# Optimization experiments

Measured on AMD Instinct MI355X. Metric: run time of the kernel, lower is better.

The kernel has to match this reference:

```python
import jax, jax.numpy as jnp
import numpy as np

N_NODES = 100000
N_EDGES = 800000
HIDDEN = 128
BN_EPS = 1e-5


def setup_inputs() -> dict:
    key = jax.random.key(0)
    k1, k2, k3 = jax.random.split(key, 3)
    x = jax.random.normal(k1, (N_NODES, HIDDEN), dtype=jnp.float32)
    edge_index = jax.random.randint(k2, (2, N_EDGES), 0, N_NODES, dtype=jnp.int64)
    # Glorot-style init for the GCN linear weight
    W = jax.random.normal(k3, (HIDDEN, HIDDEN), dtype=jnp.float32) / np.sqrt(HIDDEN)
    b = jnp.zeros((HIDDEN,), dtype=jnp.float32)
    gamma = jnp.ones((HIDDEN,), dtype=jnp.float32)
    beta = jnp.zeros((HIDDEN,), dtype=jnp.float32)
    return {"x": x, "edge_index": edge_index, "W": W, "b": b, "gamma": gamma, "beta": beta}


def reference(x, edge_index, W, b, gamma, beta):
    N = x.shape[0]
    xw = x @ W  # [N, d] linear transform first (PyG order)

    # add self-loops
    loops = jnp.arange(N, dtype=edge_index.dtype)
    row = jnp.concatenate([edge_index[0], loops])  # source
    col = jnp.concatenate([edge_index[1], loops])  # target

    # symmetric degree normalization on A~ = A + I
    deg = jax.ops.segment_sum(jnp.ones_like(col, dtype=x.dtype), col, num_segments=N)
    dinv = jax.lax.rsqrt(jnp.maximum(deg, 1.0))  # deg >= 1 due to self-loops
    norm = dinv[row] * dinv[col]  # [E+N]

    # gather -> scale -> scatter-add aggregation
    msgs = xw[row] * norm[:, None]  # [E+N, d]
    agg = jax.ops.segment_sum(msgs, col, num_segments=N) + b  # [N, d]

    # BatchNorm1d (batch statistics, biased variance) + ReLU; Dropout is identity (eval)
    mean = jnp.mean(agg, axis=0)
    var = jnp.var(agg, axis=0)
    h = (agg - mean) * jax.lax.rsqrt(var + BN_EPS) * gamma + beta
    return jax.nn.relu(h)
```

## Files before the change

### kernel.cpp

```cpp
#include <hip/hip_runtime.h>
#include <cstddef>

#define HIDDEN 128
#define BN_EPS 1e-5f
#define KS 136
#define BKT 64

typedef __attribute__((ext_vector_type(8))) short short8;
typedef __attribute__((ext_vector_type(4))) float float4v;
typedef __attribute__((ext_vector_type(4))) unsigned uint4v;

__device__ inline unsigned bf16_rne(float f) {
    unsigned u = __float_as_uint(f);
    return (u + 0x7fff + ((u >> 16) & 1)) >> 16;
}
__device__ inline unsigned pack2_bf16(float a, float b) {
    return bf16_rne(a) | (bf16_rne(b) << 16);
}
__device__ inline short8 pack8_bf16(float4 a, float4 b) {
    union { unsigned u[4]; short8 s; } t;
    t.u[0] = pack2_bf16(a.x, a.y);
    t.u[1] = pack2_bf16(a.z, a.w);
    t.u[2] = pack2_bf16(b.x, b.y);
    t.u[3] = pack2_bf16(b.z, b.w);
    return t.s;
}

__global__ __launch_bounds__(256, 4) void k_front(const float* __restrict__ x,
                                                  const float* __restrict__ W,
                                                  unsigned short* __restrict__ xus,
                                                  const int* __restrict__ col,
                                                  const int* __restrict__ row,
                                                  int* __restrict__ cnt, int* bucket,
                                                  int N, int E, int GB, int CB) {
    __shared__ unsigned short lB[128 * KS];
    int bid = blockIdx.x;
    int tid = threadIdx.x;
    int m2 = 2 * (GB < CB ? GB : CB);
    bool isGemm;
    int rid;
    if (bid < m2) {
        isGemm = (bid & 1);
        rid = bid >> 1;
    } else {
        isGemm = (GB > CB);
        rid = (m2 >> 1) + (bid - m2);
    }

    if (!isGemm) {
        int e = rid * 256 + tid;
        if (e < E) {
            int c = col[e];
            int r = row[e];
            int p = atomicAdd(&cnt[c], 1);
            if (p < BKT) bucket[(size_t)c * BKT + p] = r;
        }
        return;
    }

    int row0 = rid * 128;
    int wv = tid >> 6;
    int lane = tid & 63;
    int l15 = lane & 15;
    int lq = lane >> 4;

    for (int it = 0; it < 16; ++it) {
        int idx4 = it * 256 + tid;
        int k = idx4 >> 5, n4 = idx4 & 31;
        float4 v = ((const float4*)W)[(size_t)k * 32 + n4];
        int n = n4 * 4;
        lB[(n + 0) * KS + k] = (unsigned short)bf16_rne(v.x);
        lB[(n + 1) * KS + k] = (unsigned short)bf16_rne(v.y);
        lB[(n + 2) * KS + k] = (unsigned short)bf16_rne(v.z);
        lB[(n + 3) * KS + k] = (unsigned short)bf16_rne(v.w);
    }
    __syncthreads();

    float4v acc[2][8];
#pragma unroll
    for (int i = 0; i < 2; ++i)
#pragma unroll
        for (int j = 0; j < 8; ++j) acc[i][j] = (float4v){0.f, 0.f, 0.f, 0.f};

    int r0g = row0 + wv * 32 + l15;
    int r1g = r0g + 16;
    const float4 z4 = make_float4(0.f, 0.f, 0.f, 0.f);

#pragma unroll
    for (int kc = 0; kc < 4; ++kc) {
        int ko = kc * 32 + lq * 8;
        const float4* xr0 = (const float4*)x + (size_t)r0g * 32 + (ko >> 2);
        const float4* xr1 = (const float4*)x + (size_t)r1g * 32 + (ko >> 2);
        float4 v00 = (r0g < N) ? xr0[0] : z4;
        float4 v01 = (r0g < N) ? xr0[1] : z4;
        float4 v10 = (r1g < N) ? xr1[0] : z4;
        float4 v11 = (r1g < N) ? xr1[1] : z4;
        short8 a0 = pack8_bf16(v00, v01);
        short8 a1 = pack8_bf16(v10, v11);
        short8 bfr[8];
#pragma unroll
        for (int nt = 0; nt < 8; ++nt)
            bfr[nt] = *(const short8*)&lB[(nt * 16 + l15) * KS + ko];
#pragma unroll
        for (int nt = 0; nt < 8; ++nt) {
            acc[0][nt] = __builtin_amdgcn_mfma_f32_16x16x32_bf16(a0, bfr[nt], acc[0][nt], 0, 0, 0);
            acc[1][nt] = __builtin_amdgcn_mfma_f32_16x16x32_bf16(a1, bfr[nt], acc[1][nt], 0, 0, 0);
        }
    }

    __syncthreads();

#pragma unroll
    for (int mt = 0; mt < 2; ++mt) {
#pragma unroll
        for (int reg = 0; reg < 4; ++reg) {
            int rl = wv * 32 + mt * 16 + lq * 4 + reg;
#pragma unroll
            for (int nt = 0; nt < 8; ++nt)
                lB[rl * KS + nt * 16 + l15] = (unsigned short)bf16_rne(acc[mt][nt][reg]);
        }
    }
    __syncthreads();

    for (int it = 0; it < 8; ++it) {
        int idx = it * 256 + tid;
        int r = idx >> 4, c16 = idx & 15;
        int grow = row0 + r;
        if (grow < N) {
            uint4v v = *(const uint4v*)&lB[r * KS + c16 * 8];
            *((uint4v*)(xus + (size_t)grow * 128) + c16) = v;
        }
    }
}

__global__ __launch_bounds__(256) void k_gather(const unsigned* __restrict__ xu,
                                                const int* __restrict__ cnt,
                                                const float* __restrict__ b,
                                                unsigned* aggsrc,
                                                float* __restrict__ bn, int N) {
    int tid = threadIdx.x;
    int lane = tid & 63;
    int w = (blockIdx.x * 256 + tid) >> 6;
    int nw = (gridDim.x * 256) >> 6;
    float2 bb = ((const float2*)b)[lane];
    float2 s = make_float2(0.f, 0.f), qq = make_float2(0.f, 0.f);

    const int* bkt = (const int*)aggsrc;

    int i = w;
    int deg = 0;
    unsigned uself = 0;
    int pf[16];
#pragma unroll
    for (int k = 0; k < 16; ++k) pf[k] = 0;
    if (i < N) {
        deg = cnt[i];
        uself = xu[(size_t)i * 64 + lane];
        const int4* bp = (const int4*)(bkt + (size_t)i * BKT);
        int4 q0 = bp[0], q1 = bp[1], q2 = bp[2], q3 = bp[3];
        pf[0] = q0.x; pf[1] = q0.y; pf[2]  = q0.z; pf[3]  = q0.w;
        pf[4] = q1.x; pf[5] = q1.y; pf[6]  = q1.z; pf[7]  = q1.w;
        pf[8] = q2.x; pf[9] = q2.y; pf[10] = q2.z; pf[11] = q2.w;
        pf[12] = q3.x; pf[13] = q3.y; pf[14] = q3.z; pf[15] = q3.w;
    }

    while (i < N) {
        int inext = i + nw;
        int ndeg = 0;
        unsigned nself = 0;
        int npf[16];
#pragma unroll
        for (int k = 0; k < 16; ++k) npf[k] = 0;
        if (inext < N) {
            ndeg = cnt[inext];
            nself = xu[(size_t)inext * 64 + lane];
            const int4* bp = (const int4*)(bkt + (size_t)inext * BKT);
            int4 q0 = bp[0], q1 = bp[1], q2 = bp[2], q3 = bp[3];
            npf[0] = q0.x; npf[1] = q0.y; npf[2]  = q0.z; npf[3]  = q0.w;
            npf[4] = q1.x; npf[5] = q1.y; npf[6]  = q1.z; npf[7]  = q1.w;
            npf[8] = q2.x; npf[9] = q2.y; npf[10] = q2.z; npf[11] = q2.w;
            npf[12] = q3.x; npf[13] = q3.y; npf[14] = q3.z; npf[15] = q3.w;
        }

        int d = __builtin_amdgcn_readfirstlane(deg);
        if (d > BKT) d = BKT;
        float di = rsqrtf((float)(d + 1));
        float ax = __uint_as_float(uself << 16) * di;
        float ay = __uint_as_float(uself & 0xffff0000u) * di;

        if (d > 0) {
            int rks[8];
            unsigned u[8];
            float ds[8];
#pragma unroll
            for (int k = 0; k < 8; ++k) rks[k] = (k < d) ? pf[k] : pf[0];
#pragma unroll
            for (int k = 0; k < 8; ++k) u[k] = xu[(size_t)rks[k] * 64 + lane];
#pragma unroll
            for (int k = 0; k < 8; ++k) ds[k] = rsqrtf((float)(cnt[rks[k]] + 1));
#pragma unroll
            for (int k = 0; k < 8; ++k) {
                unsigned uu = (k < d) ? u[k] : 0u;
                ax = fmaf(__uint_as_float(uu << 16), ds[k], ax);
                ay = fmaf(__uint_as_float(uu & 0xffff0000u), ds[k], ay);
            }
        }
        if (d > 8) {
            int rks[8];
            unsigned u[8];
            float ds[8];
#pragma unroll
            for (int k = 0; k < 8; ++k) rks[k] = (8 + k < d) ? pf[8 + k] : pf[0];
#pragma unroll
            for (int k = 0; k < 8; ++k) u[k] = xu[(size_t)rks[k] * 64 + lane];
#pragma unroll
            for (int k = 0; k < 8; ++k) ds[k] = rsqrtf((float)(cnt[rks[k]] + 1));
#pragma unroll
            for (int k = 0; k < 8; ++k) {
                unsigned uu = (8 + k < d) ? u[k] : 0u;
                ax = fmaf(__uint_as_float(uu << 16), ds[k], ax);
                ay = fmaf(__uint_as_float(uu & 0xffff0000u), ds[k], ay);
            }
        }
        if (d > 16) {
            const int* bp = bkt + (size_t)i * BKT;
            int j = 16;
            for (; j + 8 <= d; j += 8) {
                int rr[8];
                unsigned u[8];
                float ds[8];
#pragma unroll
                for (int k = 0; k < 8; ++k) rr[k] = bp[j + k];
#pragma unroll
                for (int k = 0; k < 8; ++k) u[k] = xu[(size_t)rr[k] * 64 + lane];
#pragma unroll
                for (int k = 0; k < 8; ++k) ds[k] = rsqrtf((float)(cnt[rr[k]] + 1));
#pragma unroll
                for (int k = 0; k < 8; ++k) {
                    ax = fmaf(__uint_as_float(u[k] << 16), ds[k], ax);
                    ay = fmaf(__uint_as_float(u[k] & 0xffff0000u), ds[k], ay);
                }
            }
            if (j < d) {
                int last = d - 1;
                int rr[7];
                unsigned u[7];
                float ds[7];
#pragma unroll
                for (int k = 0; k < 7; ++k) {
                    int jk = j + k;
                    rr[k] = bp[jk < d ? jk : last];
                }
#pragma unroll
                for (int k = 0; k < 7; ++k) u[k] = xu[(size_t)rr[k] * 64 + lane];
#pragma unroll
                for (int k = 0; k < 7; ++k) ds[k] = rsqrtf((float)(cnt[rr[k]] + 1));
#pragma unroll
                for (int k = 0; k < 7; ++k) {
                    unsigned uu = (j + k < d) ? u[k] : 0u;
                    ax = fmaf(__uint_as_float(uu << 16), ds[k], ax);
                    ay = fmaf(__uint_as_float(uu & 0xffff0000u), ds[k], ay);
                }
            }
        }

        float ox = fmaf(ax, di, bb.x);
        float oy = fmaf(ay, di, bb.y);
        aggsrc[(size_t)i * 64 + lane] = pack2_bf16(ox, oy);
        s.x += ox;
        s.y += oy;
        qq.x = fmaf(ox, ox, qq.x);
        qq.y = fmaf(oy, oy, qq.y);

        i = inext;
        deg = ndeg;
        uself = nself;
#pragma unroll
        for (int k = 0; k < 16; ++k) pf[k] = npf[k];
    }

    __shared__ float ssum[HIDDEN];
    __shared__ float ssq[HIDDEN];
    if (tid < HIDDEN) { ssum[tid] = 0.f; ssq[tid] = 0.f; }
    __syncthreads();
    atomicAdd(&ssum[2 * lane],     s.x);
    atomicAdd(&ssum[2 * lane + 1], s.y);
    atomicAdd(&ssq[2 * lane],      qq.x);
    atomicAdd(&ssq[2 * lane + 1],  qq.y);
    __syncthreads();
    if (tid < HIDDEN) {
        atomicAdd(&bn[tid],          ssum[tid]);
        atomicAdd(&bn[HIDDEN + tid], ssq[tid]);
    }
}

__global__ __launch_bounds__(256) void k_apply(const unsigned* __restrict__ agg,
                                               float* __restrict__ out,
                                               const float* __restrict__ bn,
                                               const float* __restrict__ gamma,
                                               const float* __restrict__ beta,
                                               int total8, float invN) {
    __shared__ float sc[HIDDEN], sh[HIDDEN];
    int tid = threadIdx.x;
    if (tid < HIDDEN) {
        float mean = bn[tid] * invN;
        float var = bn[HIDDEN + tid] * invN - mean * mean;
        float inv = rsqrtf(var + BN_EPS);
        float g = gamma[tid] * inv;
        sc[tid] = g;
        sh[tid] = beta[tid] - mean * g;
    }
    __syncthreads();
    int idx = blockIdx.x * 256 + tid;
    if (idx < total8) {
        uint2 u = ((const uint2*)agg)[idx];
        int c = (idx & 31) * 4;
        float4 v;
        v.x = __uint_as_float(u.x << 16);
        v.y = __uint_as_float(u.x & 0xffff0000u);
        v.z = __uint_as_float(u.y << 16);
        v.w = __uint_as_float(u.y & 0xffff0000u);
        v.x = fmaxf(fmaf(v.x, sc[c],     sh[c]),     0.f);
        v.y = fmaxf(fmaf(v.y, sc[c + 1], sh[c + 1]), 0.f);
        v.z = fmaxf(fmaf(v.z, sc[c + 2], sh[c + 2]), 0.f);
        v.w = fmaxf(fmaf(v.w, sc[c + 3], sh[c + 3]), 0.f);
        ((float4*)out)[idx] = v;
    }
}

extern "C" void kernel_launch(void* const* d_in, const int* in_sizes, int n_in,
                              void* d_out, int out_size, void* d_ws, size_t ws_size,
                              hipStream_t stream) {
    const float* x     = (const float*)d_in[0];
    const int*   edges = (const int*)d_in[1];
    const float* W     = (const float*)d_in[2];
    const float* b     = (const float*)d_in[3];
    const float* gamma = (const float*)d_in[4];
    const float* beta  = (const float*)d_in[5];
    float* out = (float*)d_out;

    int N = in_sizes[0] / HIDDEN;
    int E = in_sizes[1] / 2;
    const int* row = edges;
    const int* col = edges + E;

    char* p = (char*)d_ws;
    unsigned* xu  = (unsigned*)p; p += (size_t)N * 64 * sizeof(unsigned);
    unsigned* agg = (unsigned*)p; p += (size_t)N * 64 * sizeof(unsigned);
    int*   cnt    = (int*)p;   p += (size_t)N * sizeof(int);
    float* bn     = (float*)p; p += 256 * sizeof(float);

    size_t zbytes = (size_t)N * sizeof(int) + 256 * sizeof(float);

    int GB = (N + 127) / 128;
    int CB = (E + 255) / 256;

    dim3 blk(256);
    hipMemsetAsync(cnt, 0, zbytes, stream);
    k_front<<<dim3(GB + CB), blk, 0, stream>>>(x, W, (unsigned short*)xu, col, row,
                                               cnt, (int*)agg, N, E, GB, CB);
    k_gather<<<dim3(2048), blk, 0, stream>>>(xu, cnt, b, agg, bn, N);
    int total8 = N * 32;
    k_apply<<<dim3((total8 + 255) / 256), blk, 0, stream>>>(agg, out, bn, gamma, beta,
                                                            total8, 1.0f / (float)N);
}
```

Before: 261.3 us.

## Pretranspose W once, shrink GEMM LDS staging, add dynamic node scheduling in gather

A new zero kernel replaces the memset and also converts W to a transposed bf16 copy once, so each GEMM block reads B fragments straight from global/L2 instead of rebuilding a 34KB LDS tile. The output staging now uses a small 40-column LDS buffer written in four column groups, which raises occupancy at the cost of extra barriers. The gather kernel switches from static strided node assignment to an atomic work cursor handing out chunks of four nodes, meant to balance degree skew. The risks are atomic contention on the cursor and uncoalesced global B-fragment loads.

```diff
diff --git a/kernel.cpp b/kernel.cpp
--- a/kernel.cpp
+++ b/kernel.cpp
@@ -3,8 +3,8 @@
 
 #define HIDDEN 128
 #define BN_EPS 1e-5f
-#define KS 136
 #define BKT 64
+#define CS 40
 
 typedef __attribute__((ext_vector_type(8))) short short8;
 typedef __attribute__((ext_vector_type(4))) float float4v;
@@ -26,14 +26,26 @@
     return t.s;
 }
 
+__global__ __launch_bounds__(256) void k_zero(int* __restrict__ z, int nz,
+                                              const float* __restrict__ W,
+                                              unsigned short* __restrict__ wtb) {
+    int t = blockIdx.x * 256 + threadIdx.x;
+    int nthr = gridDim.x * 256;
+    for (int i = t; i < nz; i += nthr) z[i] = 0;
+    for (int i = t; i < HIDDEN * HIDDEN; i += nthr) {
+        int k = i >> 7, n = i & 127;
+        wtb[n * 128 + k] = (unsigned short)bf16_rne(W[i]);
+    }
+}
+
 __global__ __launch_bounds__(256, 4) void k_front(const float* __restrict__ x,
-                                                  const float* __restrict__ W,
+                                                  const unsigned short* __restrict__ wtb,
                                                   unsigned short* __restrict__ xus,
                                                   const int* __restrict__ col,
                                                   const int* __restrict__ row,
                                                   int* __restrict__ cnt, int* bucket,
                                                   int N, int E, int GB, int CB) {
-    __shared__ unsigned short lB[128 * KS];
+    __shared__ unsigned short lC[128 * CS];
     int bid = blockIdx.x;
     int tid = threadIdx.x;
     int m2 = 2 * (GB < CB ? GB : CB);
@@ -64,18 +76,6 @@
     int l15 = lane & 15;
     int lq = lane >> 4;
 
-    for (int it = 0; it < 16; ++it) {
-        int idx4 = it * 256 + tid;
-        int k = idx4 >> 5, n4 = idx4 & 31;
-        float4 v = ((const float4*)W)[(size_t)k * 32 + n4];
-        int n = n4 * 4;
-        lB[(n + 0) * KS + k] = (unsigned short)bf16_rne(v.x);
-        lB[(n + 1) * KS + k] = (unsigned short)bf16_rne(v.y);
-        lB[(n + 2) * KS + k] = (unsigned short)bf16_rne(v.z);
-        lB[(n + 3) * KS + k] = (unsigned short)bf16_rne(v.w);
-    }
-    __syncthreads();
-
     float4v acc[2][8];
 #pragma unroll
     for (int i = 0; i < 2; ++i)
@@ -100,7 +100,7 @@
         short8 bfr[8];
 #pragma unroll
         for (int nt = 0; nt < 8; ++nt)
-            bfr[nt] = *(const short8*)&lB[(nt * 16 + l15) * KS + ko];
+            bfr[nt] = *(const short8*)&wtb[(nt * 16 + l15) * 128 + ko];
 #pragma unroll
         for (int nt = 0; nt < 8; ++nt) {
             acc[0][nt] = __builtin_amdgcn_mfma_f32_16x16x32_bf16(a0, bfr[nt], acc[0][nt], 0, 0, 0);
@@ -108,27 +108,27 @@
         }
     }
 
-    __syncthreads();
-
-#pragma unroll
-    for (int mt = 0; mt < 2; ++mt) {
-#pragma unroll
-        for (int reg = 0; reg < 4; ++reg) {
-            int rl = wv * 32 + mt * 16 + lq * 4 + reg;
-#pragma unroll
-            for (int nt = 0; nt < 8; ++nt)
-                lB[rl * KS + nt * 16 + l15] = (unsigned short)bf16_rne(acc[mt][nt][reg]);
-        }
-    }
-    __syncthreads();
-
-    for (int it = 0; it < 8; ++it) {
-        int idx = it * 256 + tid;
-        int r = idx >> 4, c16 = idx & 15;
-        int grow = row0 + r;
-        if (grow < N) {
-            uint4v v = *(const uint4v*)&lB[r * KS + c16 * 8];
-            *((uint4v*)(xus + (size_t)grow * 128) + c16) = v;
+#pragma unroll
+    for (int g = 0; g < 4; ++g) {
+        if (g) __syncthreads();
+#pragma unroll
+        for (int mt = 0; mt < 2; ++mt)
+#pragma unroll
+            for (int reg = 0; reg < 4; ++reg) {
+                int rl = wv * 32 + mt * 16 + lq * 4 + reg;
+#pragma unroll
+                for (int nt2 = 0; nt2 < 2; ++nt2)
+                    lC[rl * CS + nt2 * 16 + l15] =
+                        (unsigned short)bf16_rne(acc[mt][g * 2 + nt2][reg]);
+            }
+        __syncthreads();
+        for (int it = 0; it < 2; ++it) {
+            int idx = it * 256 + tid;
+            int r = idx >> 2, c4 = idx & 3;
+            int grow = row0 + r;
+            if (grow < N)
+                *((uint4v*)(xus + (size_t)grow * 128 + g * 32) + c4) =
+                    *(const uint4v*)&lC[r * CS + c4 * 8];
         }
     }
 }
@@ -137,17 +137,23 @@
                                                 const int* __restrict__ cnt,
                                                 const float* __restrict__ b,
                                                 unsigned* aggsrc,
-                                                float* __restrict__ bn, int N) {
+                                                float* __restrict__ bn,
+                                                int* __restrict__ cursor, int N) {
     int tid = threadIdx.x;
     int lane = tid & 63;
-    int w = (blockIdx.x * 256 + tid) >> 6;
-    int nw = (gridDim.x * 256) >> 6;
     float2 bb = ((const float2*)b)[lane];
     float2 s = make_float2(0.f, 0.f), qq = make_float2(0.f, 0.f);
 
     const int* bkt = (const int*)aggsrc;
 
-    int i = w;
+    int g0 = 0, g1 = 0;
+    if (lane == 0) g0 = atomicAdd(cursor, 4);
+    int base = __builtin_amdgcn_readfirstlane(g0);
+    if (lane == 0) g1 = atomicAdd(cursor, 4);
+    int pend = __builtin_amdgcn_readfirstlane(g1);
+    int slot = 0;
+
+    int i = base;
     int deg = 0;
     unsigned uself = 0;
     int pf[16];
@@ -165,7 +171,19 @@
     }
 
     while (i < N) {
-        int inext = i + nw;
+        int inext;
+        if (slot == 3) {
+            inext = pend;
+            base = pend;
+            int gn = 0;
+            if (lane == 0) gn = atomicAdd(cursor, 4);
+            pend = __builtin_amdgcn_readfirstlane(gn);
+            slot = 0;
+        } else {
+            inext = base + slot + 1;
+            ++slot;
+        }
+
         int ndeg = 0;
         unsigned nself = 0;
         int npf[16];
@@ -349,17 +367,19 @@
     unsigned* agg = (unsigned*)p; p += (size_t)N * 64 * sizeof(unsigned);
     int*   cnt    = (int*)p;   p += (size_t)N * sizeof(int);
     float* bn     = (float*)p; p += 256 * sizeof(float);
-
-    size_t zbytes = (size_t)N * sizeof(int) + 256 * sizeof(float);
+    int*   cursor = (int*)p;   p += 4 * sizeof(int);
+    unsigned short* wtb = (unsigned short*)p; p += HIDDEN * HIDDEN * sizeof(unsigned short);
+
+    int nz = N + 256 + 4;
 
     int GB = (N + 127) / 128;
     int CB = (E + 255) / 256;
 
     dim3 blk(256);
-    hipMemsetAsync(cnt, 0, zbytes, stream);
-    k_front<<<dim3(GB + CB), blk, 0, stream>>>(x, W, (unsigned short*)xu, col, row,
+    k_zero<<<dim3(256), blk, 0, stream>>>(cnt, nz, W, wtb);
+    k_front<<<dim3(GB + CB), blk, 0, stream>>>(x, wtb, (unsigned short*)xu, col, row,
                                                cnt, (int*)agg, N, E, GB, CB);
-    k_gather<<<dim3(2048), blk, 0, stream>>>(xu, cnt, b, agg, bn, N);
+    k_gather<<<dim3(2048), blk, 0, stream>>>(xu, cnt, b, agg, bn, cursor, N);
     int total8 = N * 32;
     k_apply<<<dim3((total8 + 255) / 256), blk, 0, stream>>>(agg, out, bn, gamma, beta,
                                                             total8, 1.0f / (float)N);
```

New measurement: 691.7 us. 2.65x slower.
